# Optimization experiments

Measured on AMD Instinct MI355X. Metric: run time of the kernel, lower is better.

The kernel has to match this reference:

```python
import jax, jax.numpy as jnp
import numpy as np

N, F, P, E, HID = 50000, 4, 12, 1_600_000, 64  # nodes, input feats, periods (FH), edges, hidden


def setup_inputs() -> dict:
    key = jax.random.key(0)
    ks = jax.random.split(key, 16)

    def nrm(k, shp, scale=0.1):
        return jax.random.normal(k, shp, jnp.float32) * scale

    inp = {
        "x": jax.random.normal(ks[0], (N, F, P), jnp.float32),
        "edge_index": jax.random.randint(ks[1], (2, E), 0, N),
        "edge_weights": jax.random.uniform(ks[2], (E,), jnp.float32),
        "att": nrm(ks[3], (P,), 1.0),
    }
    i = 4
    for g in ("z", "r", "h"):  # TGCN gate params: GCNConv weight/bias + Linear(2*hid, hid)
        inp[f"Wg_{g}"] = nrm(ks[i], (F, HID))
        inp[f"bg_{g}"] = jnp.zeros((HID,), jnp.float32)
        inp[f"Wl_{g}"] = nrm(jax.random.fold_in(ks[i], 1), (2 * HID, HID))
        inp[f"bl_{g}"] = jnp.zeros((HID,), jnp.float32)
        i += 1
    for j in range(1, 5):
        inp[f"W{j}"] = nrm(ks[i], (HID, HID))
        inp[f"b{j}"] = jnp.zeros((HID,), jnp.float32)
        i += 1
    inp["Wo"] = nrm(ks[i], (HID, P * F))
    inp["bo"] = jnp.zeros((P * F,), jnp.float32)
    return inp


def _gcn_norm(edge_index, ew):
    # GCNConv default: add self loops (weight 1), symmetric D^-1/2 (A+I) D^-1/2 normalization
    src, dst = edge_index[0], edge_index[1]
    loop = jnp.arange(N)
    src_f = jnp.concatenate([src, loop])
    dst_f = jnp.concatenate([dst, loop])
    ew_f = jnp.concatenate([ew, jnp.ones((N,), ew.dtype)])
    deg = jax.ops.segment_sum(ew_f, dst_f, num_segments=N)
    dinv = jnp.where(deg > 0, jax.lax.rsqrt(deg), 0.0)
    norm = dinv[src_f] * ew_f * dinv[dst_f]
    return src_f, dst_f, norm


def _gcn(x, W, b, src, dst, norm):
    xw = x @ W                               # [N, HID] transform before propagate
    msg = xw[src] * norm[:, None]            # gather + scale, [E+N, HID]
    return jax.ops.segment_sum(msg, dst, num_segments=N) + b


def reference(x, edge_index, edge_weights, att,
              Wg_z, bg_z, Wl_z, bl_z,
              Wg_r, bg_r, Wl_r, bl_r,
              Wg_h, bg_h, Wl_h, bl_h,
              W1, b1, W2, b2, W3, b3, W4, b4, Wo, bo):
    src, dst, norm = _gcn_norm(edge_index, edge_weights)

    def tgcn_cell(xt):
        # A3TGCN passes H=None every period -> H starts at zeros each period
        Hz = jnp.zeros((xt.shape[0], HID), xt.dtype)
        z = jax.nn.sigmoid(jnp.concatenate([_gcn(xt, Wg_z, bg_z, src, dst, norm), Hz], -1) @ Wl_z + bl_z)
        r = jax.nn.sigmoid(jnp.concatenate([_gcn(xt, Wg_r, bg_r, src, dst, norm), Hz], -1) @ Wl_r + bl_r)
        htil = jnp.tanh(jnp.concatenate([_gcn(xt, Wg_h, bg_h, src, dst, norm), Hz * r], -1) @ Wl_h + bl_h)
        return z * Hz + (1.0 - z) * htil

    probs = jax.nn.softmax(att)
    h = jnp.zeros((N, HID), x.dtype)
    for p in range(P):  # small fixed period loop keeps peak memory at one period's messages
        h = h + probs[p] * tgcn_cell(x[:, :, p])

    h = jax.nn.relu(h)
    h = h @ W1 + b1
    h = h @ W2 + b2
    h = h @ W3 + b3
    h = h @ W4 + b4
    h = h @ Wo + bo                          # [N, FH*F]
    return h.reshape(-1, F, P)
```

## Files before the change

kernel.cpp:

```cpp
#include <hip/hip_runtime.h>
#include <hip/hip_fp16.h>

#define FP 48
#define HID 64
#define NP 12
#define PL 65
#define NBB 256
#define BT 1024
#define SEGW 72
#define SPAN (NBB * SEGW)
#define CSRCAP 9216

__device__ __forceinline__ void mm_stage(const float* __restrict__ Alds,
                                         const float* __restrict__ Wg,
                                         float* __restrict__ Clds, int t)
{
    const int rg = (t >> 4) * 4, cg = (t & 15) * 4;
    float acc[4][4] = {};
    for (int k = 0; k < 64; ++k) {
        float a0 = Alds[(rg + 0) * PL + k];
        float a1 = Alds[(rg + 1) * PL + k];
        float a2 = Alds[(rg + 2) * PL + k];
        float a3 = Alds[(rg + 3) * PL + k];
        const float4 bv = *reinterpret_cast<const float4*>(Wg + k * 64 + cg);
        acc[0][0] += a0 * bv.x; acc[0][1] += a0 * bv.y; acc[0][2] += a0 * bv.z; acc[0][3] += a0 * bv.w;
        acc[1][0] += a1 * bv.x; acc[1][1] += a1 * bv.y; acc[1][2] += a1 * bv.z; acc[1][3] += a1 * bv.w;
        acc[2][0] += a2 * bv.x; acc[2][1] += a2 * bv.y; acc[2][2] += a2 * bv.z; acc[2][3] += a2 * bv.w;
        acc[3][0] += a3 * bv.x; acc[3][1] += a3 * bv.y; acc[3][2] += a3 * bv.z; acc[3][3] += a3 * bv.w;
    }
    for (int i = 0; i < 4; ++i)
        for (int j = 0; j < 4; ++j)
            Clds[(rg + i) * PL + cg + j] = acc[i][j];
}

__device__ __forceinline__ void bias_stage(const float* __restrict__ bin,
                                           const float* __restrict__ Wg,
                                           const float* __restrict__ badd,
                                           float* __restrict__ bout, int t)
{
    if (t < 64) {
        float s = badd[t];
        for (int k = 0; k < 64; ++k) s += bin[k] * Wg[k * 64 + t];
        bout[t] = s;
    }
}

__device__ void do_prep(
    const float* __restrict__ att,
    const float* __restrict__ Wg_z, const float* __restrict__ bg_z,
    const float* __restrict__ Wl_z, const float* __restrict__ bl_z,
    const float* __restrict__ Wg_h, const float* __restrict__ bg_h,
    const float* __restrict__ Wl_h, const float* __restrict__ bl_h,
    const float* __restrict__ W1, const float* __restrict__ b1,
    const float* __restrict__ W2, const float* __restrict__ b2,
    const float* __restrict__ W3, const float* __restrict__ b3,
    const float* __restrict__ W4, const float* __restrict__ b4,
    const float* __restrict__ Wo, const float* __restrict__ bo,
    float* __restrict__ probs, float* __restrict__ Mz, float* __restrict__ cz,
    float* __restrict__ Mh, float* __restrict__ ch,
    float* __restrict__ Wc, float* __restrict__ bc,
    float* __restrict__ smem, int t)
{
    float* A     = smem;
    float* B     = smem + 4160;
    float* bias  = smem + 8320;
    float* bias2 = smem + 8384;

    if (t == 0) {
        float m = att[0];
        for (int p = 1; p < NP; ++p) m = fmaxf(m, att[p]);
        float e[NP]; float s = 0.f;
        for (int p = 0; p < NP; ++p) { e[p] = __expf(att[p] - m); s += e[p]; }
        float inv = 1.f / s;
        for (int p = 0; p < NP; ++p) probs[p] = e[p] * inv;
    }

    if (t < 256) {
        int f = t >> 6, j = t & 63;
        float az = 0.f, ah = 0.f;
        for (int k = 0; k < HID; ++k) {
            az += Wg_z[f * HID + k] * Wl_z[k * HID + j];
            ah += Wg_h[f * HID + k] * Wl_h[k * HID + j];
        }
        Mz[t] = az; Mh[t] = ah;
    }
    if (t < HID) {
        float az = bl_z[t], ah = bl_h[t];
        for (int k = 0; k < HID; ++k) {
            az += bg_z[k] * Wl_z[k * HID + t];
            ah += bg_h[k] * Wl_h[k * HID + t];
        }
        cz[t] = az; ch[t] = ah;
    }

    for (int idx = t; idx < 4096; idx += BT) {
        int i = idx >> 6, j = idx & 63;
        A[i * PL + j] = W1[idx];
    }
    if (t < 64) bias[t] = b1[t];
    __syncthreads();

    if (t < 256) mm_stage(A, W2, B, t);
    bias_stage(bias, W2, b2, bias2, t);
    __syncthreads();
    if (t < 256) mm_stage(B, W3, A, t);
    bias_stage(bias2, W3, b3, bias, t);
    __syncthreads();
    if (t < 256) mm_stage(A, W4, B, t);
    bias_stage(bias, W4, b4, bias2, t);
    __syncthreads();

    if (t < 256) {
        const int rg = (t >> 4) * 4, cg = (t & 15) * 4;
        if (cg < FP) {
            float acc[4][4] = {};
            for (int k = 0; k < 64; ++k) {
                float a0 = B[(rg + 0) * PL + k];
                float a1 = B[(rg + 1) * PL + k];
                float a2 = B[(rg + 2) * PL + k];
                float a3 = B[(rg + 3) * PL + k];
                const float4 bv = *reinterpret_cast<const float4*>(Wo + k * FP + cg);
                acc[0][0] += a0 * bv.x; acc[0][1] += a0 * bv.y; acc[0][2] += a0 * bv.z; acc[0][3] += a0 * bv.w;
                acc[1][0] += a1 * bv.x; acc[1][1] += a1 * bv.y; acc[1][2] += a1 * bv.z; acc[1][3] += a1 * bv.w;
                acc[2][0] += a2 * bv.x; acc[2][1] += a2 * bv.y; acc[2][2] += a2 * bv.z; acc[2][3] += a2 * bv.w;
                acc[3][0] += a3 * bv.x; acc[3][1] += a3 * bv.y; acc[3][2] += a3 * bv.z; acc[3][3] += a3 * bv.w;
            }
            for (int i = 0; i < 4; ++i)
                for (int j = 0; j < 4; ++j)
                    Wc[(rg + i) * FP + cg + j] = acc[i][j];
        }
        if (t < FP) {
            float s = bo[t];
            for (int k = 0; k < 64; ++k) s += bias2[k] * Wo[k * FP + t];
            bc[t] = s;
        }
    }
}

__global__ __launch_bounds__(BT) void build_kernel(
    const int* __restrict__ src, const int* __restrict__ dst,
    const float* __restrict__ ew,
    unsigned short* __restrict__ cnts16, int2* __restrict__ binned,
    int E, int CE, int NBUK,
    const float* __restrict__ att,
    const float* __restrict__ Wg_z, const float* __restrict__ bg_z,
    const float* __restrict__ Wl_z, const float* __restrict__ bl_z,
    const float* __restrict__ Wg_h, const float* __restrict__ bg_h,
    const float* __restrict__ Wl_h, const float* __restrict__ bl_h,
    const float* __restrict__ W1, const float* __restrict__ b1,
    const float* __restrict__ W2, const float* __restrict__ b2,
    const float* __restrict__ W3, const float* __restrict__ b3,
    const float* __restrict__ W4, const float* __restrict__ b4,
    const float* __restrict__ Wo, const float* __restrict__ bo,
    float* __restrict__ probs, float* __restrict__ Mz, float* __restrict__ cz,
    float* __restrict__ Mh, float* __restrict__ ch,
    float* __restrict__ Wc, float* __restrict__ bc)
{
    __shared__ __align__(16) float smem[8448];
    const int t = threadIdx.x;
    const int bid = blockIdx.x;

    if (bid == NBB) {
        do_prep(att, Wg_z, bg_z, Wl_z, bl_z, Wg_h, bg_h, Wl_h, bl_h,
                W1, b1, W2, b2, W3, b3, W4, b4, Wo, bo,
                probs, Mz, cz, Mh, ch, Wc, bc, smem, t);
        return;
    }

    int* cnt = (int*)smem;
    const int base = bid * CE;
    for (int i = t; i < NBUK; i += BT) cnt[i] = 0;
    __syncthreads();

    for (int g = t; 4 * g < CE; g += BT) {
        const int e0 = base + 4 * g;
        if (e0 + 3 < E) {
            const int4 d4 = *reinterpret_cast<const int4*>(dst + e0);
            atomicAdd(&cnt[((unsigned)d4.x) >> 8], 1);
            atomicAdd(&cnt[((unsigned)d4.y) >> 8], 1);
            atomicAdd(&cnt[((unsigned)d4.z) >> 8], 1);
            atomicAdd(&cnt[((unsigned)d4.w) >> 8], 1);
        } else {
            for (int j = 0; j < 4; ++j)
                if (e0 + j < E)
                    atomicAdd(&cnt[((unsigned)dst[e0 + j]) >> 8], 1);
        }
    }
    __syncthreads();

    for (int i = t; i < NBUK; i += BT)
        cnts16[i * NBB + bid] = (unsigned short)min(cnt[i], SEGW);
    __syncthreads();
    for (int i = t; i < NBUK; i += BT) cnt[i] = 0;
    __syncthreads();

    for (int g = t; 4 * g < CE; g += BT) {
        const int e0 = base + 4 * g;
        if (e0 + 3 < E) {
            const int4   d4 = *reinterpret_cast<const int4*>(dst + e0);
            const int4   s4 = *reinterpret_cast<const int4*>(src + e0);
            const float4 w4 = *reinterpret_cast<const float4*>(ew + e0);
            {
                const int bk = ((unsigned)d4.x) >> 8;
                const int r = atomicAdd(&cnt[bk], 1);
                if (r < SEGW) binned[(size_t)bk * SPAN + bid * SEGW + r] =
                    make_int2(((d4.x & 255) << 16) | s4.x, __float_as_int(w4.x));
            }
            {
                const int bk = ((unsigned)d4.y) >> 8;
                const int r = atomicAdd(&cnt[bk], 1);
                if (r < SEGW) binned[(size_t)bk * SPAN + bid * SEGW + r] =
                    make_int2(((d4.y & 255) << 16) | s4.y, __float_as_int(w4.y));
            }
            {
                const int bk = ((unsigned)d4.z) >> 8;
                const int r = atomicAdd(&cnt[bk], 1);
                if (r < SEGW) binned[(size_t)bk * SPAN + bid * SEGW + r] =
                    make_int2(((d4.z & 255) << 16) | s4.z, __float_as_int(w4.z));
            }
            {
                const int bk = ((unsigned)d4.w) >> 8;
                const int r = atomicAdd(&cnt[bk], 1);
                if (r < SEGW) binned[(size_t)bk * SPAN + bid * SEGW + r] =
                    make_int2(((d4.w & 255) << 16) | s4.w, __float_as_int(w4.w));
            }
        } else {
            for (int j = 0; j < 4; ++j) {
                const int e = e0 + j;
                if (e < E) {
                    const int d = dst[e];
                    const int bk = ((unsigned)d) >> 8;
                    const int r = atomicAdd(&cnt[bk], 1);
                    if (r < SEGW) binned[(size_t)bk * SPAN + bid * SEGW + r] =
                        make_int2(((d & 255) << 16) | src[e], __float_as_int(ew[e]));
                }
            }
        }
    }
}

__global__ __launch_bounds__(BT) void csr_convert_kernel(
    const unsigned short* __restrict__ cnts16, const int2* __restrict__ binned,
    unsigned* __restrict__ csr, int2* __restrict__ nodeinfo,
    const float* __restrict__ x, unsigned short* __restrict__ xs,
    int N, int NBUK)
{
    __shared__ int   scnt[256];
    __shared__ int   ccnt[256];
    __shared__ float cfsum[256];
    __shared__ int   cpfx[256];
    __shared__ float csdi[256];

    const int t = threadIdx.x;
    const int b = blockIdx.x;
    const int node0 = b << 8;
    const int nend = min(256, N - node0);
    const size_t sb = (size_t)b * SPAN;

    if (t < 256) {
        scnt[t] = (int)cnts16[b * NBB + t];
        ccnt[t] = 0; cfsum[t] = 0.f;
    }
    __syncthreads();

    for (int i = t; i < SPAN; i += BT) {
        const int seg = (int)((unsigned)i / (unsigned)SEGW);
        const int j = i - seg * SEGW;
        if (j < scnt[seg]) {
            const int2 v = binned[sb + i];
            const int dl = (v.x >> 16) & 255;
            atomicAdd(&ccnt[dl], 1);
            atomicAdd(&cfsum[dl], __int_as_float(v.y));
        }
    }
    __syncthreads();

    const int myc = (t < 256) ? ccnt[t] : 0;
    if (t < 256) cpfx[t] = myc;
    __syncthreads();
    for (int off = 1; off < 256; off <<= 1) {
        int tmp = 0;
        if (t < 256 && t >= off) tmp = cpfx[t - off];
        __syncthreads();
        if (t < 256 && t >= off) cpfx[t] += tmp;
        __syncthreads();
    }

    const int ebeg = b * CSRCAP;
    if (t < 256) {
        const int excl = cpfx[t] - myc;
        const float di = rsqrtf(1.f + cfsum[t]);
        csdi[t] = di;
        if (t < nend)
            nodeinfo[node0 + t] =
                make_int2((myc << 22) | (ebeg + excl), __float_as_int(di));
        ccnt[t] = ebeg + excl;
    }
    __syncthreads();

    for (int i = t; i < SPAN; i += BT) {
        const int seg = (int)((unsigned)i / (unsigned)SEGW);
        const int j = i - seg * SEGW;
        if (j < scnt[seg]) {
            const int2 v = binned[sb + i];
            const int dl = (v.x >> 16) & 255;
            const int pos = atomicAdd(&ccnt[dl], 1);
            const float w = __int_as_float(v.y);
            const unsigned hb = (unsigned)__half_as_ushort(__float2half_rn(w));
            csr[pos] = (unsigned)(v.x & 0xffff) | (hb << 16);
        }
    }

    const int gtot = nend * 6;
    for (int g = t; g < gtot; g += BT) {
        const int nl = g / 6;
        const int q = g - nl * 6;
        const float dsc = csdi[nl];
        const float* xr = x + (size_t)(node0 + nl) * FP + q * 8;
        const float4 v0 = *reinterpret_cast<const float4*>(xr);
        const float4 v1 = *reinterpret_cast<const float4*>(xr + 4);
        unsigned p0 = (unsigned)__half_as_ushort(__float2half_rn(dsc * v0.x)) |
                      ((unsigned)__half_as_ushort(__float2half_rn(dsc * v0.y)) << 16);
        unsigned p1 = (unsigned)__half_as_ushort(__float2half_rn(dsc * v0.z)) |
                      ((unsigned)__half_as_ushort(__float2half_rn(dsc * v0.w)) << 16);
        unsigned p2 = (unsigned)__half_as_ushort(__float2half_rn(dsc * v1.x)) |
                      ((unsigned)__half_as_ushort(__float2half_rn(dsc * v1.y)) << 16);
        unsigned p3 = (unsigned)__half_as_ushort(__float2half_rn(dsc * v1.z)) |
                      ((unsigned)__half_as_ushort(__float2half_rn(dsc * v1.w)) << 16);
        *reinterpret_cast<int4*>(xs + (size_t)(node0 + nl) * FP + q * 8) =
            make_int4((int)p0, (int)p1, (int)p2, (int)p3);
    }
}

__global__ __launch_bounds__(256) void gather_node_kernel(
    const unsigned short* __restrict__ xs, const float* __restrict__ x,
    const int2* __restrict__ nodeinfo,
    const unsigned* __restrict__ csr,
    const float* __restrict__ probs,
    const float* __restrict__ Mz, const float* __restrict__ cz,
    const float* __restrict__ Mh, const float* __restrict__ ch,
    const float* __restrict__ Wc, const float* __restrict__ bc,
    float* __restrict__ out, int N)
{
    __shared__ __align__(16) float sWc[HID * FP];
    __shared__ __align__(16) float sprobs[16];
    __shared__ __align__(16) float yacc[4][384];
    __shared__ __align__(16) float yld[4][FP];
    __shared__ __align__(16) float hld[4][HID];
    for (int i = threadIdx.x; i < HID * FP; i += 256) sWc[i] = Wc[i];
    if (threadIdx.x < NP) sprobs[threadIdx.x] = probs[threadIdx.x];
    __syncthreads();

    const int lane = threadIdx.x & 63;
    const int wib  = threadIdx.x >> 6;
    const int n    = blockIdx.x * 4 + wib;
    if (n >= N) return;

    const int slot = lane >> 3;
    const int q    = lane & 7;
    const bool act = (q < 6);
    const int qc   = act ? q : 5;
    const char* xsb = (const char*)xs;

    const int2 ni = nodeinfo[n];
    const int beg = ni.x & 0x3FFFFF;
    const int end = beg + (int)((unsigned)ni.x >> 22);
    const float di = __int_as_float(ni.y);

    float a0 = 0.f, a1 = 0.f, a2 = 0.f, a3 = 0.f;
    float a4 = 0.f, a5 = 0.f, a6 = 0.f, a7 = 0.f;
    #pragma unroll 2
    for (int e = beg + slot; e < end; e += 8) {
        const unsigned ev = csr[e];
        const float w = __half2float(__ushort_as_half((unsigned short)(ev >> 16)));
        const unsigned soff = (ev & 0xffffu) * 96u;
        const int4 xv = *reinterpret_cast<const int4*>(xsb + soff + (qc << 4));
        const float2 f0 = __half22float2(*reinterpret_cast<const __half2*>(&xv.x));
        const float2 f1 = __half22float2(*reinterpret_cast<const __half2*>(&xv.y));
        const float2 f2 = __half22float2(*reinterpret_cast<const __half2*>(&xv.z));
        const float2 f3 = __half22float2(*reinterpret_cast<const __half2*>(&xv.w));
        a0 = fmaf(w, f0.x, a0); a1 = fmaf(w, f0.y, a1);
        a2 = fmaf(w, f1.x, a2); a3 = fmaf(w, f1.y, a3);
        a4 = fmaf(w, f2.x, a4); a5 = fmaf(w, f2.y, a5);
        a6 = fmaf(w, f3.x, a6); a7 = fmaf(w, f3.y, a7);
    }

    if (act) {
        float* dst0 = &yacc[wib][slot * 48 + q * 8];
        *reinterpret_cast<float4*>(dst0)     = make_float4(a0, a1, a2, a3);
        *reinterpret_cast<float4*>(dst0 + 4) = make_float4(a4, a5, a6, a7);
    }

    if (lane < FP) {
        const float* yf = yacc[wib];
        float s = 0.f;
        #pragma unroll
        for (int sl = 0; sl < 8; ++sl) s += yf[sl * 48 + lane];
        float xself = x[(size_t)n * FP + lane];
        float yv = di * s + di * di * xself;
        int f = lane / 12;
        int p = lane - f * 12;
        yld[wib][p * 4 + f] = yv;
    }

    const float mz0 = Mz[lane], mz1 = Mz[64 + lane], mz2 = Mz[128 + lane], mz3 = Mz[192 + lane];
    const float mh0 = Mh[lane], mh1 = Mh[64 + lane], mh2 = Mh[128 + lane], mh3 = Mh[192 + lane];
    const float czv = cz[lane], chv = ch[lane];
    const int   c   = (lane < FP) ? lane : 0;
    const float bcv = bc[c];

    const float* yw = yld[wib];
    float hacc = 0.f;
    #pragma unroll
    for (int p = 0; p < NP; ++p) {
        const float4 v = *reinterpret_cast<const float4*>(yw + p * 4);
        float az = czv + v.x * mz0 + v.y * mz1 + v.z * mz2 + v.w * mz3;
        float ah = chv + v.x * mh0 + v.y * mh1 + v.z * mh2 + v.w * mh3;
        float g  = __builtin_amdgcn_rcpf(1.f + __expf(az));
        float ahc = fminf(fmaxf(ah, -15.f), 15.f);
        float eh = __expf(2.f * ahc);
        float th = 1.f - 2.f * __builtin_amdgcn_rcpf(eh + 1.f);
        hacc += sprobs[p] * g * th;
    }
    hacc = fmaxf(hacc, 0.f);

    hld[wib][lane] = hacc;
    const float* hw = hld[wib];
    float o = bcv;
    #pragma unroll
    for (int i4 = 0; i4 < 16; ++i4) {
        const float4 h4 = *reinterpret_cast<const float4*>(hw + i4 * 4);
        o += h4.x * sWc[(i4 * 4 + 0) * FP + c];
        o += h4.y * sWc[(i4 * 4 + 1) * FP + c];
        o += h4.z * sWc[(i4 * 4 + 2) * FP + c];
        o += h4.w * sWc[(i4 * 4 + 3) * FP + c];
    }
    if (lane < FP) out[(size_t)n * FP + lane] = o;
}

extern "C" void kernel_launch(void* const* d_in, const int* in_sizes, int n_in,
                              void* d_out, int out_size, void* d_ws, size_t ws_size,
                              hipStream_t stream)
{
    const int N = in_sizes[0] / FP;
    const int E = in_sizes[1] / 2;
    const int NBUK = (N + 255) >> 8;
    const int CE = (((E + NBB - 1) / NBB) + 3) & ~3;

    const float* x    = (const float*)d_in[0];
    const int*   ei   = (const int*)d_in[1];
    const float* ew   = (const float*)d_in[2];
    const float* att  = (const float*)d_in[3];
    const float* Wg_z = (const float*)d_in[4];
    const float* bg_z = (const float*)d_in[5];
    const float* Wl_z = (const float*)d_in[6];
    const float* bl_z = (const float*)d_in[7];
    const float* Wg_h = (const float*)d_in[12];
    const float* bg_h = (const float*)d_in[13];
    const float* Wl_h = (const float*)d_in[14];
    const float* bl_h = (const float*)d_in[15];
    const float* W1 = (const float*)d_in[16]; const float* b1 = (const float*)d_in[17];
    const float* W2 = (const float*)d_in[18]; const float* b2 = (const float*)d_in[19];
    const float* W3 = (const float*)d_in[20]; const float* b3 = (const float*)d_in[21];
    const float* W4 = (const float*)d_in[22]; const float* b4 = (const float*)d_in[23];
    const float* Wo = (const float*)d_in[24]; const float* bo = (const float*)d_in[25];

    const int* srcp = ei;
    const int* dstp = ei + E;

    int2* binned        = (int2*)d_ws;
    unsigned* csr       = (unsigned*)(binned + (size_t)NBUK * SPAN);
    unsigned short* xs  = (unsigned short*)(csr + (size_t)NBUK * CSRCAP);
    unsigned short* cnts16 = (unsigned short*)(xs + (size_t)N * FP);
    int2* nodeinfo      = (int2*)(cnts16 + (size_t)NBUK * NBB + 128);
    float* probs        = (float*)(nodeinfo + N);
    float* Mz           = probs + 16;
    float* cz           = Mz + 256;
    float* Mh           = cz + 64;
    float* ch           = Mh + 256;
    float* Wc           = ch + 64;
    float* bc           = Wc + HID * FP;

    build_kernel<<<NBB + 1, BT, 0, stream>>>(
        srcp, dstp, ew, cnts16, binned, E, CE, NBUK,
        att, Wg_z, bg_z, Wl_z, bl_z, Wg_h, bg_h, Wl_h, bl_h,
        W1, b1, W2, b2, W3, b3, W4, b4, Wo, bo,
        probs, Mz, cz, Mh, ch, Wc, bc);

    csr_convert_kernel<<<NBUK, BT, 0, stream>>>(cnts16, binned, csr, nodeinfo,
                                                x, xs, N, NBUK);

    gather_node_kernel<<<(N + 3) / 4, 256, 0, stream>>>(xs, x, nodeinfo, csr,
                                                        probs, Mz, cz, Mh, ch, Wc, bc,
                                                        (float*)d_out, N);
}
```

Before: 264.9 us.

## Drop CSR conversion; aggregate binned edges directly with LDS atomics per bucket

The build kernel now scatters edges into 128-node buckets in one pass, deriving per-segment counts from the scatter counters instead of a separate counting pass. The CSR build is replaced by a degree-only histogram kernel that writes dinv and the scaled fp16 features. The gather kernel now runs one 1024-thread block per bucket: it reads the binned edges directly and accumulates messages into a shared-memory tile with float atomics, then runs the per-node gate and output math. This removes one pass over dst, the CSR write and reread, and the per-node index table. In exchange it relies on LDS float atomic throughput, and float summation order is no longer deterministic.

```diff
diff --git a/kernel.cpp b/kernel.cpp
--- a/kernel.cpp
+++ b/kernel.cpp
@@ -7,9 +7,10 @@
 #define PL 65
 #define NBB 256
 #define BT 1024
-#define SEGW 72
+#define BKN 128
+#define SEGW 48
 #define SPAN (NBB * SEGW)
-#define CSRCAP 9216
+#define YP 49
 
 __device__ __forceinline__ void mm_stage(const float* __restrict__ Alds,
                                          const float* __restrict__ Wg,
@@ -137,7 +138,7 @@
     }
 }
 
-__global__ __launch_bounds__(BT) void build_kernel(
+__global__ __launch_bounds__(BT, 8) void build_kernel(
     const int* __restrict__ src, const int* __restrict__ dst,
     const float* __restrict__ ew,
     unsigned short* __restrict__ cnts16, int2* __restrict__ binned,
@@ -175,147 +176,95 @@
     for (int g = t; 4 * g < CE; g += BT) {
         const int e0 = base + 4 * g;
         if (e0 + 3 < E) {
-            const int4 d4 = *reinterpret_cast<const int4*>(dst + e0);
-            atomicAdd(&cnt[((unsigned)d4.x) >> 8], 1);
-            atomicAdd(&cnt[((unsigned)d4.y) >> 8], 1);
-            atomicAdd(&cnt[((unsigned)d4.z) >> 8], 1);
-            atomicAdd(&cnt[((unsigned)d4.w) >> 8], 1);
-        } else {
-            for (int j = 0; j < 4; ++j)
-                if (e0 + j < E)
-                    atomicAdd(&cnt[((unsigned)dst[e0 + j]) >> 8], 1);
-        }
-    }
-    __syncthreads();
-
-    for (int i = t; i < NBUK; i += BT)
-        cnts16[i * NBB + bid] = (unsigned short)min(cnt[i], SEGW);
-    __syncthreads();
-    for (int i = t; i < NBUK; i += BT) cnt[i] = 0;
-    __syncthreads();
-
-    for (int g = t; 4 * g < CE; g += BT) {
-        const int e0 = base + 4 * g;
-        if (e0 + 3 < E) {
             const int4   d4 = *reinterpret_cast<const int4*>(dst + e0);
             const int4   s4 = *reinterpret_cast<const int4*>(src + e0);
             const float4 w4 = *reinterpret_cast<const float4*>(ew + e0);
             {
-                const int bk = ((unsigned)d4.x) >> 8;
+                const int bk = ((unsigned)d4.x) >> 7;
                 const int r = atomicAdd(&cnt[bk], 1);
                 if (r < SEGW) binned[(size_t)bk * SPAN + bid * SEGW + r] =
-                    make_int2(((d4.x & 255) << 16) | s4.x, __float_as_int(w4.x));
+                    make_int2(((d4.x & 127) << 16) | s4.x, __float_as_int(w4.x));
             }
             {
-                const int bk = ((unsigned)d4.y) >> 8;
+                const int bk = ((unsigned)d4.y) >> 7;
                 const int r = atomicAdd(&cnt[bk], 1);
                 if (r < SEGW) binned[(size_t)bk * SPAN + bid * SEGW + r] =
-                    make_int2(((d4.y & 255) << 16) | s4.y, __float_as_int(w4.y));
+                    make_int2(((d4.y & 127) << 16) | s4.y, __float_as_int(w4.y));
             }
             {
-                const int bk = ((unsigned)d4.z) >> 8;
+                const int bk = ((unsigned)d4.z) >> 7;
                 const int r = atomicAdd(&cnt[bk], 1);
                 if (r < SEGW) binned[(size_t)bk * SPAN + bid * SEGW + r] =
-                    make_int2(((d4.z & 255) << 16) | s4.z, __float_as_int(w4.z));
+                    make_int2(((d4.z & 127) << 16) | s4.z, __float_as_int(w4.z));
             }
             {
-                const int bk = ((unsigned)d4.w) >> 8;
+                const int bk = ((unsigned)d4.w) >> 7;
                 const int r = atomicAdd(&cnt[bk], 1);
                 if (r < SEGW) binned[(size_t)bk * SPAN + bid * SEGW + r] =
-                    make_int2(((d4.w & 255) << 16) | s4.w, __float_as_int(w4.w));
+                    make_int2(((d4.w & 127) << 16) | s4.w, __float_as_int(w4.w));
             }
         } else {
             for (int j = 0; j < 4; ++j) {
                 const int e = e0 + j;
                 if (e < E) {
                     const int d = dst[e];
-                    const int bk = ((unsigned)d) >> 8;
+                    const int bk = ((unsigned)d) >> 7;
                     const int r = atomicAdd(&cnt[bk], 1);
                     if (r < SEGW) binned[(size_t)bk * SPAN + bid * SEGW + r] =
-                        make_int2(((d & 255) << 16) | src[e], __float_as_int(ew[e]));
+                        make_int2(((d & 127) << 16) | src[e], __float_as_int(ew[e]));
                 }
             }
         }
     }
-}
-
-__global__ __launch_bounds__(BT) void csr_convert_kernel(
+    __syncthreads();
+
+    for (int i = t; i < NBUK; i += BT)
+        cnts16[i * NBB + bid] = (unsigned short)min(cnt[i], SEGW);
+}
+
+__global__ __launch_bounds__(BT, 8) void hist_convert_kernel(
     const unsigned short* __restrict__ cnts16, const int2* __restrict__ binned,
-    unsigned* __restrict__ csr, int2* __restrict__ nodeinfo,
-    const float* __restrict__ x, unsigned short* __restrict__ xs,
-    int N, int NBUK)
+    float* __restrict__ dinv, const float* __restrict__ x,
+    unsigned short* __restrict__ xs, int N, int NBUK)
 {
     __shared__ int   scnt[256];
-    __shared__ int   ccnt[256];
-    __shared__ float cfsum[256];
-    __shared__ int   cpfx[256];
-    __shared__ float csdi[256];
+    __shared__ float fsum[BKN];
+    __shared__ float sdi[BKN];
 
     const int t = threadIdx.x;
     const int b = blockIdx.x;
-    const int node0 = b << 8;
-    const int nend = min(256, N - node0);
+    const int node0 = b * BKN;
+    const int nend = min(BKN, N - node0);
     const size_t sb = (size_t)b * SPAN;
 
-    if (t < 256) {
-        scnt[t] = (int)cnts16[b * NBB + t];
-        ccnt[t] = 0; cfsum[t] = 0.f;
-    }
-    __syncthreads();
-
-    for (int i = t; i < SPAN; i += BT) {
-        const int seg = (int)((unsigned)i / (unsigned)SEGW);
-        const int j = i - seg * SEGW;
-        if (j < scnt[seg]) {
-            const int2 v = binned[sb + i];
-            const int dl = (v.x >> 16) & 255;
-            atomicAdd(&ccnt[dl], 1);
-            atomicAdd(&cfsum[dl], __int_as_float(v.y));
-        }
-    }
-    __syncthreads();
-
-    const int myc = (t < 256) ? ccnt[t] : 0;
-    if (t < 256) cpfx[t] = myc;
-    __syncthreads();
-    for (int off = 1; off < 256; off <<= 1) {
-        int tmp = 0;
-        if (t < 256 && t >= off) tmp = cpfx[t - off];
-        __syncthreads();
-        if (t < 256 && t >= off) cpfx[t] += tmp;
-        __syncthreads();
-    }
-
-    const int ebeg = b * CSRCAP;
-    if (t < 256) {
-        const int excl = cpfx[t] - myc;
-        const float di = rsqrtf(1.f + cfsum[t]);
-        csdi[t] = di;
-        if (t < nend)
-            nodeinfo[node0 + t] =
-                make_int2((myc << 22) | (ebeg + excl), __float_as_int(di));
-        ccnt[t] = ebeg + excl;
-    }
-    __syncthreads();
-
-    for (int i = t; i < SPAN; i += BT) {
-        const int seg = (int)((unsigned)i / (unsigned)SEGW);
-        const int j = i - seg * SEGW;
-        if (j < scnt[seg]) {
-            const int2 v = binned[sb + i];
-            const int dl = (v.x >> 16) & 255;
-            const int pos = atomicAdd(&ccnt[dl], 1);
-            const float w = __int_as_float(v.y);
-            const unsigned hb = (unsigned)__half_as_ushort(__float2half_rn(w));
-            csr[pos] = (unsigned)(v.x & 0xffff) | (hb << 16);
-        }
-    }
+    if (t < 256) scnt[t] = (int)cnts16[b * NBB + t];
+    if (t < BKN) fsum[t] = 0.f;
+    __syncthreads();
+
+    {
+        const int seg = t >> 2;
+        const int sub = t & 3;
+        const int c = scnt[seg];
+        const size_t segbase = sb + (size_t)seg * SEGW;
+        for (int j = sub; j < c; j += 4) {
+            const int2 v = binned[segbase + j];
+            atomicAdd(&fsum[(v.x >> 16) & 127], __int_as_float(v.y));
+        }
+    }
+    __syncthreads();
+
+    if (t < BKN) {
+        const float di = rsqrtf(1.f + fsum[t]);
+        sdi[t] = di;
+        if (t < nend) dinv[node0 + t] = di;
+    }
+    __syncthreads();
 
     const int gtot = nend * 6;
     for (int g = t; g < gtot; g += BT) {
         const int nl = g / 6;
         const int q = g - nl * 6;
-        const float dsc = csdi[nl];
+        const float dsc = sdi[nl];
         const float* xr = x + (size_t)(node0 + nl) * FP + q * 8;
         const float4 v0 = *reinterpret_cast<const float4*>(xr);
         const float4 v1 = *reinterpret_cast<const float4*>(xr + 4);
@@ -332,110 +281,121 @@
     }
 }
 
-__global__ __launch_bounds__(256) void gather_node_kernel(
+__global__ __launch_bounds__(BT, 8) void gather_node_kernel(
     const unsigned short* __restrict__ xs, const float* __restrict__ x,
-    const int2* __restrict__ nodeinfo,
-    const unsigned* __restrict__ csr,
+    const float* __restrict__ dinv,
+    const unsigned short* __restrict__ cnts16, const int2* __restrict__ binned,
     const float* __restrict__ probs,
     const float* __restrict__ Mz, const float* __restrict__ cz,
     const float* __restrict__ Mh, const float* __restrict__ ch,
     const float* __restrict__ Wc, const float* __restrict__ bc,
-    float* __restrict__ out, int N)
+    float* __restrict__ out, int N, int NBUK)
 {
     __shared__ __align__(16) float sWc[HID * FP];
     __shared__ __align__(16) float sprobs[16];
-    __shared__ __align__(16) float yacc[4][384];
-    __shared__ __align__(16) float yld[4][FP];
-    __shared__ __align__(16) float hld[4][HID];
-    for (int i = threadIdx.x; i < HID * FP; i += 256) sWc[i] = Wc[i];
-    if (threadIdx.x < NP) sprobs[threadIdx.x] = probs[threadIdx.x];
-    __syncthreads();
-
-    const int lane = threadIdx.x & 63;
-    const int wib  = threadIdx.x >> 6;
-    const int n    = blockIdx.x * 4 + wib;
-    if (n >= N) return;
-
+    __shared__ __align__(16) float y[BKN * YP];
+    __shared__ __align__(16) float yld[16][FP];
+    __shared__ __align__(16) float hld[16][HID];
+    __shared__ int   scnt[256];
+    __shared__ float sdi[BKN];
+
+    const int t = threadIdx.x;
+    const int b = blockIdx.x;
+    const int node0 = b * BKN;
+    const int nend = min(BKN, N - node0);
+    const size_t sb = (size_t)b * SPAN;
+
+    for (int i = t; i < HID * FP; i += BT) sWc[i] = Wc[i];
+    if (t < NP) sprobs[t] = probs[t];
+    if (t < 256) scnt[t] = (int)cnts16[b * NBB + t];
+    if (t < BKN) sdi[t] = dinv[node0 + t];
+    for (int i = t; i < BKN * YP; i += BT) y[i] = 0.f;
+    __syncthreads();
+
+    const int lane = t & 63;
+    const int wib  = t >> 6;
     const int slot = lane >> 3;
     const int q    = lane & 7;
     const bool act = (q < 6);
     const int qc   = act ? q : 5;
     const char* xsb = (const char*)xs;
 
-    const int2 ni = nodeinfo[n];
-    const int beg = ni.x & 0x3FFFFF;
-    const int end = beg + (int)((unsigned)ni.x >> 22);
-    const float di = __int_as_float(ni.y);
-
-    float a0 = 0.f, a1 = 0.f, a2 = 0.f, a3 = 0.f;
-    float a4 = 0.f, a5 = 0.f, a6 = 0.f, a7 = 0.f;
-    #pragma unroll 2
-    for (int e = beg + slot; e < end; e += 8) {
-        const unsigned ev = csr[e];
-        const float w = __half2float(__ushort_as_half((unsigned short)(ev >> 16)));
-        const unsigned soff = (ev & 0xffffu) * 96u;
-        const int4 xv = *reinterpret_cast<const int4*>(xsb + soff + (qc << 4));
-        const float2 f0 = __half22float2(*reinterpret_cast<const __half2*>(&xv.x));
-        const float2 f1 = __half22float2(*reinterpret_cast<const __half2*>(&xv.y));
-        const float2 f2 = __half22float2(*reinterpret_cast<const __half2*>(&xv.z));
-        const float2 f3 = __half22float2(*reinterpret_cast<const __half2*>(&xv.w));
-        a0 = fmaf(w, f0.x, a0); a1 = fmaf(w, f0.y, a1);
-        a2 = fmaf(w, f1.x, a2); a3 = fmaf(w, f1.y, a3);
-        a4 = fmaf(w, f2.x, a4); a5 = fmaf(w, f2.y, a5);
-        a6 = fmaf(w, f3.x, a6); a7 = fmaf(w, f3.y, a7);
-    }
-
-    if (act) {
-        float* dst0 = &yacc[wib][slot * 48 + q * 8];
-        *reinterpret_cast<float4*>(dst0)     = make_float4(a0, a1, a2, a3);
-        *reinterpret_cast<float4*>(dst0 + 4) = make_float4(a4, a5, a6, a7);
-    }
-
-    if (lane < FP) {
-        const float* yf = yacc[wib];
-        float s = 0.f;
-        #pragma unroll
-        for (int sl = 0; sl < 8; ++sl) s += yf[sl * 48 + lane];
-        float xself = x[(size_t)n * FP + lane];
-        float yv = di * s + di * di * xself;
-        int f = lane / 12;
-        int p = lane - f * 12;
-        yld[wib][p * 4 + f] = yv;
-    }
+    for (int seg = wib; seg < NBB; seg += 16) {
+        const int c = scnt[seg];
+        const size_t segbase = sb + (size_t)seg * SEGW;
+        for (int jb = 0; jb < c; jb += 8) {
+            const int j = jb + slot;
+            if (j < c) {
+                const int2 v = binned[segbase + j];
+                const float w = __int_as_float(v.y);
+                const int dlow = (v.x >> 16) & 127;
+                const unsigned soff = ((unsigned)v.x & 0xffffu) * 96u;
+                if (act) {
+                    const int4 xv = *reinterpret_cast<const int4*>(xsb + soff + (qc << 4));
+                    const float2 f0 = __half22float2(*reinterpret_cast<const __half2*>(&xv.x));
+                    const float2 f1 = __half22float2(*reinterpret_cast<const __half2*>(&xv.y));
+                    const float2 f2 = __half22float2(*reinterpret_cast<const __half2*>(&xv.z));
+                    const float2 f3 = __half22float2(*reinterpret_cast<const __half2*>(&xv.w));
+                    float* yp = &y[dlow * YP + q * 8];
+                    atomicAdd(yp + 0, w * f0.x); atomicAdd(yp + 1, w * f0.y);
+                    atomicAdd(yp + 2, w * f1.x); atomicAdd(yp + 3, w * f1.y);
+                    atomicAdd(yp + 4, w * f2.x); atomicAdd(yp + 5, w * f2.y);
+                    atomicAdd(yp + 6, w * f3.x); atomicAdd(yp + 7, w * f3.y);
+                }
+            }
+        }
+    }
+    __syncthreads();
 
     const float mz0 = Mz[lane], mz1 = Mz[64 + lane], mz2 = Mz[128 + lane], mz3 = Mz[192 + lane];
     const float mh0 = Mh[lane], mh1 = Mh[64 + lane], mh2 = Mh[128 + lane], mh3 = Mh[192 + lane];
     const float czv = cz[lane], chv = ch[lane];
-    const int   c   = (lane < FP) ? lane : 0;
-    const float bcv = bc[c];
-
-    const float* yw = yld[wib];
-    float hacc = 0.f;
-    #pragma unroll
-    for (int p = 0; p < NP; ++p) {
-        const float4 v = *reinterpret_cast<const float4*>(yw + p * 4);
-        float az = czv + v.x * mz0 + v.y * mz1 + v.z * mz2 + v.w * mz3;
-        float ah = chv + v.x * mh0 + v.y * mh1 + v.z * mh2 + v.w * mh3;
-        float g  = __builtin_amdgcn_rcpf(1.f + __expf(az));
-        float ahc = fminf(fmaxf(ah, -15.f), 15.f);
-        float eh = __expf(2.f * ahc);
-        float th = 1.f - 2.f * __builtin_amdgcn_rcpf(eh + 1.f);
-        hacc += sprobs[p] * g * th;
-    }
-    hacc = fmaxf(hacc, 0.f);
-
-    hld[wib][lane] = hacc;
-    const float* hw = hld[wib];
-    float o = bcv;
-    #pragma unroll
-    for (int i4 = 0; i4 < 16; ++i4) {
-        const float4 h4 = *reinterpret_cast<const float4*>(hw + i4 * 4);
-        o += h4.x * sWc[(i4 * 4 + 0) * FP + c];
-        o += h4.y * sWc[(i4 * 4 + 1) * FP + c];
-        o += h4.z * sWc[(i4 * 4 + 2) * FP + c];
-        o += h4.w * sWc[(i4 * 4 + 3) * FP + c];
-    }
-    if (lane < FP) out[(size_t)n * FP + lane] = o;
+    const int   cI  = (lane < FP) ? lane : 0;
+    const float bcv = bc[cI];
+
+    for (int k = 0; k < 8; ++k) {
+        const int nl = wib * 8 + k;
+        if (nl >= nend) break;
+        const int n = node0 + nl;
+        const float di = sdi[nl];
+
+        if (lane < FP) {
+            const float yv_raw = y[nl * YP + lane];
+            const float xself = x[(size_t)n * FP + lane];
+            const float yv = di * yv_raw + di * di * xself;
+            const int f = lane / 12;
+            const int p = lane - f * 12;
+            yld[wib][p * 4 + f] = yv;
+        }
+
+        const float* yw = yld[wib];
+        float hacc = 0.f;
+        #pragma unroll
+        for (int p = 0; p < NP; ++p) {
+            const float4 v = *reinterpret_cast<const float4*>(yw + p * 4);
+            float az = czv + v.x * mz0 + v.y * mz1 + v.z * mz2 + v.w * mz3;
+            float ah = chv + v.x * mh0 + v.y * mh1 + v.z * mh2 + v.w * mh3;
+            float g  = __builtin_amdgcn_rcpf(1.f + __expf(az));
+            float ahc = fminf(fmaxf(ah, -15.f), 15.f);
+            float eh = __expf(2.f * ahc);
+            float th = 1.f - 2.f * __builtin_amdgcn_rcpf(eh + 1.f);
+            hacc += sprobs[p] * g * th;
+        }
+        hacc = fmaxf(hacc, 0.f);
+
+        hld[wib][lane] = hacc;
+        const float* hw = hld[wib];
+        float o = bcv;
+        #pragma unroll
+        for (int i4 = 0; i4 < 16; ++i4) {
+            const float4 h4 = *reinterpret_cast<const float4*>(hw + i4 * 4);
+            o += h4.x * sWc[(i4 * 4 + 0) * FP + cI];
+            o += h4.y * sWc[(i4 * 4 + 1) * FP + cI];
+            o += h4.z * sWc[(i4 * 4 + 2) * FP + cI];
+            o += h4.w * sWc[(i4 * 4 + 3) * FP + cI];
+        }
+        if (lane < FP) out[(size_t)n * FP + lane] = o;
+    }
 }
 
 extern "C" void kernel_launch(void* const* d_in, const int* in_sizes, int n_in,
@@ -444,7 +404,7 @@
 {
     const int N = in_sizes[0] / FP;
     const int E = in_sizes[1] / 2;
-    const int NBUK = (N + 255) >> 8;
+    const int NBUK = (N + BKN - 1) / BKN;
     const int CE = (((E + NBB - 1) / NBB) + 3) & ~3;
 
     const float* x    = (const float*)d_in[0];
@@ -469,11 +429,10 @@
     const int* dstp = ei + E;
 
     int2* binned        = (int2*)d_ws;
-    unsigned* csr       = (unsigned*)(binned + (size_t)NBUK * SPAN);
-    unsigned short* xs  = (unsigned short*)(csr + (size_t)NBUK * CSRCAP);
+    unsigned short* xs  = (unsigned short*)(binned + (size_t)NBUK * SPAN);
     unsigned short* cnts16 = (unsigned short*)(xs + (size_t)N * FP);
-    int2* nodeinfo      = (int2*)(cnts16 + (size_t)NBUK * NBB + 128);
-    float* probs        = (float*)(nodeinfo + N);
+    float* dinv         = (float*)(cnts16 + (size_t)NBUK * NBB + 128);
+    float* probs        = dinv + N;
     float* Mz           = probs + 16;
     float* cz           = Mz + 256;
     float* Mh           = cz + 64;
@@ -487,10 +446,9 @@
         W1, b1, W2, b2, W3, b3, W4, b4, Wo, bo,
         probs, Mz, cz, Mh, ch, Wc, bc);
 
-    csr_convert_kernel<<<NBUK, BT, 0, stream>>>(cnts16, binned, csr, nodeinfo,
-                                                x, xs, N, NBUK);
-
-    gather_node_kernel<<<(N + 3) / 4, 256, 0, stream>>>(xs, x, nodeinfo, csr,
-                                                        probs, Mz, cz, Mh, ch, Wc, bc,
-                                                        (float*)d_out, N);
-}
+    hist_convert_kernel<<<NBUK, BT, 0, stream>>>(cnts16, binned, dinv, x, xs, N, NBUK);
+
+    gather_node_kernel<<<NBUK, BT, 0, stream>>>(xs, x, dinv, cnts16, binned,
+                                                probs, Mz, cz, Mh, ch, Wc, bc,
+                                                (float*)d_out, N, NBUK);
+}
```

Result: slower. 722.0 us (+172.5%).
